# Optimization experiments

Hardware: AMD Instinct MI355X
Metric: run time of the kernel (lower is better)

## Reference

```python
import jax, jax.numpy as jnp
import numpy as np

# geomloss SamplesLoss defaults for loss='sinkhorn'
BLUR = 0.05
SCALING = 0.5
P = 1  # norm=1 -> cost C(x,y) = ||x - y||_2


def _cost(x, y):
    # Euclidean distance cost (p=1). x:(B,N,D), y:(B,M,D) -> (B,N,M)
    d2 = (jnp.sum(x * x, -1)[:, :, None]
          - 2.0 * jnp.einsum('bnd,bmd->bnm', x, y)
          + jnp.sum(y * y, -1)[:, None, :])
    return jnp.sqrt(jnp.clip(d2, 1e-12, None))  # tiny clamp keeps sqrt grad finite on diagonal


def _softmin(eps, C, h):
    # f_i = -eps * logsumexp_j( h_j - C_ij / eps );  C:(B,N,M), h:(B,M) -> (B,N)
    return -eps * jax.nn.logsumexp(h[:, None, :] - C / eps, axis=2)


def _eps_schedule(diameter):
    # geomloss epsilon_schedule(p, diameter, blur, scaling)
    return ([diameter ** P]
            + [float(np.exp(e)) for e in np.arange(P * np.log(diameter), P * np.log(BLUR), P * np.log(SCALING))]
            + [BLUR ** P])


def _sinkhorn_divergence(x, y):
    # Debiased Sinkhorn divergence (geomloss, tensorized backend, balanced OT).
    B, N, D = x.shape
    M = y.shape[1]
    a_log = jnp.full((B, N), -np.log(N), dtype=x.dtype)  # uniform weights (log)
    b_log = jnp.full((B, M), -np.log(M), dtype=x.dtype)

    C_xy = _cost(x, y)
    C_yx = jnp.swapaxes(C_xy, 1, 2)  # symmetric cost
    C_xx = _cost(x, x)
    C_yy = _cost(y, y)

    # diameter of the joint point cloud (geomloss max_diameter); concrete python float
    xf = np.asarray(x).reshape(-1, D)
    yf = np.asarray(y).reshape(-1, D)
    mins = np.minimum(xf.min(0), yf.min(0))
    maxs = np.maximum(xf.max(0), yf.max(0))
    diameter = float(np.linalg.norm(maxs - mins))
    eps_list = _eps_schedule(diameter)

    sg = jax.lax.stop_gradient

    # initialization at the largest eps
    eps = eps_list[0]
    f_aa = _softmin(eps, C_xx, a_log)
    g_bb = _softmin(eps, C_yy, b_log)
    g_ab = _softmin(eps, C_yx, a_log)
    f_ba = _softmin(eps, C_xy, b_log)

    # epsilon-annealing loop with symmetric (averaged) updates; no grad flows
    # through this loop (outputs are stop_gradient'ed in the final extrapolation)
    for eps in eps_list:
        ft_ba = _softmin(eps, C_xy, b_log + g_ab / eps)
        gt_ab = _softmin(eps, C_yx, a_log + f_ba / eps)
        f_ba = 0.5 * (f_ba + ft_ba)
        g_ab = 0.5 * (g_ab + gt_ab)
        ft_aa = _softmin(eps, C_xx, a_log + f_aa / eps)
        gt_bb = _softmin(eps, C_yy, b_log + g_bb / eps)
        f_aa = 0.5 * (f_aa + ft_aa)
        g_bb = 0.5 * (g_bb + gt_bb)

    # last extrapolation at eps = blur^p with detached dual potentials (envelope theorem)
    eps = eps_list[-1]
    f_ba_new = _softmin(eps, C_xy, sg(b_log + g_ab / eps))
    g_ab_new = _softmin(eps, C_yx, sg(a_log + f_ba / eps))
    f_aa = _softmin(eps, C_xx, sg(a_log + f_aa / eps))
    g_bb = _softmin(eps, C_yy, sg(b_log + g_bb / eps))
    f_ba, g_ab = f_ba_new, g_ab_new

    a = jnp.exp(a_log)
    b = jnp.exp(b_log)
    # S_eps(a,b) = <a, f_ba - f_aa> + <b, g_ab - g_bb>, per batch element
    return jnp.sum(a * (f_ba - f_aa), -1) + jnp.sum(b * (g_ab - g_bb), -1)


def setup_inputs() -> dict:
    key = jax.random.key(0)
    k1, k2 = jax.random.split(key)
    pre = jax.random.normal(k1, (2, 4096, 2), dtype=jnp.float32)
    gt = jax.random.normal(k2, (2, 4096, 2), dtype=jnp.float32)
    return {"pre": pre, "gt": gt}


def reference(pre, gt):
    return _sinkhorn_divergence(pre, gt).mean()
```

## Files before the change

kernel.cpp:

```cpp
#include <hip/hip_runtime.h>
#include <math.h>

#define NPTS 4096
#define NB 2
#define K_TOTAL 12
#define BLOCK 256
#define TILE 128
#define NT (NPTS / TILE)

#define SCHED_OFF 0
#define ML_OFF 32
#define P_OFF 576
#define POT_SZ (4 * NB * NPTS)
#define RED_OFF (P_OFF + 2 * POT_SZ)
#define PART_OFF (RED_OFF + 128)
#define PART_SZ (4 * NB * NT * NPTS)

#if __has_builtin(__builtin_amdgcn_exp2f)
#define EXP2F __builtin_amdgcn_exp2f
#else
#define EXP2F exp2f
#endif
#if __has_builtin(__builtin_amdgcn_logf)
#define LOG2F __builtin_amdgcn_logf
#else
#define LOG2F log2f
#endif
#if __has_builtin(__builtin_amdgcn_sqrtf)
#define FSQRTF __builtin_amdgcn_sqrtf
#else
#define FSQRTF sqrtf
#endif

#define BASE_LOGW -8.31776616671934f
#define LOG2E 1.4426950408889634f
#define LN2 0.69314718055994531f

typedef float v2f __attribute__((ext_vector_type(2)));

__global__ __launch_bounds__(256) void k_init(
    const float2* __restrict__ x, const float2* __restrict__ y, float* ws)
{
  const int tid = threadIdx.x;
  const int bid = blockIdx.x;

  if (bid > 0) {
    for (int i = (bid - 1) * 256 + tid; i < 2 * POT_SZ; i += 63 * 256)
      ws[P_OFF + i] = 0.0f;
    return;
  }

  float mnx = 1e30f, mny = 1e30f, mxx = -1e30f, mxy = -1e30f;
  for (int i = tid; i < NB * NPTS; i += 256) {
    float2 p = x[i];
    mnx = fminf(mnx, p.x); mxx = fmaxf(mxx, p.x);
    mny = fminf(mny, p.y); mxy = fmaxf(mxy, p.y);
    float2 q = y[i];
    mnx = fminf(mnx, q.x); mxx = fmaxf(mxx, q.x);
    mny = fminf(mny, q.y); mxy = fmaxf(mxy, q.y);
  }
  for (int o = 32; o; o >>= 1) {
    mnx = fminf(mnx, __shfl_xor(mnx, o, 64));
    mxx = fmaxf(mxx, __shfl_xor(mxx, o, 64));
    mny = fminf(mny, __shfl_xor(mny, o, 64));
    mxy = fmaxf(mxy, __shfl_xor(mxy, o, 64));
  }
  __shared__ float r[4][4];
  const int wave = tid >> 6, lane = tid & 63;
  if (lane == 0) { r[0][wave] = mnx; r[1][wave] = mxx; r[2][wave] = mny; r[3][wave] = mxy; }
  __syncthreads();
  if (tid == 0) {
    mnx = fminf(fminf(r[0][0], r[0][1]), fminf(r[0][2], r[0][3]));
    mxx = fmaxf(fmaxf(r[1][0], r[1][1]), fmaxf(r[1][2], r[1][3]));
    mny = fminf(fminf(r[2][0], r[2][1]), fminf(r[2][2], r[2][3]));
    mxy = fmaxf(fmaxf(r[3][0], r[3][1]), fmaxf(r[3][2], r[3][3]));
    float rx = mxx - mnx, ry = mxy - mny;
    float dia = sqrtf(rx * rx + ry * ry);

    double a = log((double)dia);
    double stop = log(0.05);
    double stp = log(0.5);
    int cnt = (int)ceil((stop - a) / stp);
    if (cnt < 0) cnt = 0;
    if (cnt > K_TOTAL - 4) cnt = K_TOTAL - 4;

    float* sch = ws + SCHED_OFF;
    sch[0] = dia; sch[1] = 0.0f;
    sch[2] = dia; sch[3] = 0.5f;
    for (int k = 0; k < cnt; k++) {
      sch[2 * (2 + k)] = (float)exp(a + (double)k * stp);
      sch[2 * (2 + k) + 1] = 0.5f;
    }
    sch[2 * (2 + cnt)] = 0.05f; sch[2 * (2 + cnt) + 1] = 0.5f;
    for (int s = 3 + cnt; s < K_TOTAL - 1; s++) { sch[2 * s] = 0.05f; sch[2 * s + 1] = 1.0f; }
    sch[2 * (K_TOTAL - 1)] = 0.05f; sch[2 * (K_TOTAL - 1) + 1] = 0.0f;
  }
}

__global__ __launch_bounds__(BLOCK, 4) void k_tiles(
    const float2* __restrict__ xpts, const float2* __restrict__ ypts,
    float* __restrict__ ws, int stepi)
{
  __shared__ float rXs[TILE], rYs[TILE], rVs[TILE];
  __shared__ float cXs[144], cYs[144], cVs[144];
  __shared__ float tPart[16][129];
  __shared__ float sfb[2][32];
  __shared__ float smx[2];
  __shared__ float wmax[4];

  const int tid = threadIdx.x;
  const int id = blockIdx.x;

  const float2* rowp; const float2* colp;
  int ti, tj, pbr, pbc;
  bool dual;

  if (id < NB * NT * NT) {
    const int b = id >> 10;
    const int t = id & (NT * NT - 1);
    ti = t >> 5; tj = t & (NT - 1);
    rowp = xpts + b * NPTS; colp = ypts + b * NPTS;
    pbr = 0 * NB + b; pbc = 1 * NB + b;
    dual = true;
  } else {
    const int id2 = id - NB * NT * NT;
    const int mat = id2 / 1056;
    const int rem = id2 - mat * 1056;
    const int b = rem / 528;
    const int k = rem - b * 528;
    int t0 = (int)((65.0f - FSQRTF((float)(4225 - 8 * k))) * 0.5f);
    while (t0 * (65 - t0) / 2 > k) t0--;
    while ((t0 + 1) * (64 - t0) / 2 <= k) t0++;
    ti = t0; tj = t0 + (k - t0 * (65 - t0) / 2);
    const float2* pts = mat ? ypts : xpts;
    rowp = pts + b * NPTS; colp = rowp;
    pbr = (2 + mat) * NB + b; pbc = pbr;
    dual = (ti != tj);
  }

  const float eps = ws[SCHED_OFF + 2 * stepi];
  const float sc = LOG2E / eps;
  const float inv_eps = 1.0f / eps;
  const int ppar = (stepi - 1) & 1;
  const int cpar = stepi & 1;

  if (stepi > 0 && tid < 64) {
    const int c = tid & 31, side = tid >> 5;
    const int pb_own = side ? pbc : pbr;
    const int spb = (pb_own < 4) ? (pb_own ^ 2) : pb_own;
    float ml = ws[ML_OFF + ppar * 256 + spb * NT + c];
    float mm = ml;
    mm = fmaxf(mm, __shfl_xor(mm, 1, 64));
    mm = fmaxf(mm, __shfl_xor(mm, 2, 64));
    mm = fmaxf(mm, __shfl_xor(mm, 4, 64));
    mm = fmaxf(mm, __shfl_xor(mm, 8, 64));
    mm = fmaxf(mm, __shfl_xor(mm, 16, 64));
    sfb[side][c] = EXP2F((ml - mm) * LOG2E);
    if (c == 0) smx[side] = mm;
  }
  __syncthreads();

  const int side = tid >> 7, kk0 = tid & 127;
  const int pb_own = side ? pbc : pbr;
  const int tile_own = side ? tj : ti;
  const int r = tile_own * TILE + kk0;
  float2 pt = (side ? colp : rowp)[r];

  float h;
  if (stepi == 0) {
    h = BASE_LOGW;
  } else {
    const float eps_p = ws[SCHED_OFF + 2 * (stepi - 1)];
    const float w_p = ws[SCHED_OFF + 2 * (stepi - 1) + 1];
    const float* pprev = ws + PART_OFF + ppar * PART_SZ + (pb_own * NT) * NPTS + r;
    float s = 0.0f;
#pragma unroll
    for (int c = 0; c < NT; c++) s += pprev[c * NPTS] * sfb[side][c];
    s = fmaxf(s, 1e-37f);
    float ft = -eps_p * fmaf(LN2, LOG2F(s), smx[side]);
    float po = ws[P_OFF + cpar * POT_SZ + pb_own * NPTS + r];
    float pn = (w_p >= 1.0f) ? po : fmaf(w_p, po, (1.0f - w_p) * ft);
    ws[P_OFF + ppar * POT_SZ + pb_own * NPTS + r] = pn;
    h = fmaf(pn, inv_eps, BASE_LOGW);
  }

  float hm = h;
  for (int o = 32; o; o >>= 1) hm = fmaxf(hm, __shfl_xor(hm, o, 64));
  if ((tid & 63) == 0) wmax[tid >> 6] = hm;
  __syncthreads();
  const float Mloc = fmaxf(wmax[2 * side], wmax[2 * side + 1]);

  if (side == 0) {
    rXs[kk0] = pt.x * sc; rYs[kk0] = pt.y * sc;
    rVs[kk0] = EXP2F((h - Mloc) * LOG2E);
  } else {
    const int kk = kk0 + (kk0 >> 3);
    cXs[kk] = pt.x * sc; cYs[kk] = pt.y * sc;
    cVs[kk] = EXP2F((h - Mloc) * LOG2E);
  }
  if (kk0 == 0) ws[ML_OFF + cpar * 256 + pb_own * NT + tile_own] = Mloc;
  __syncthreads();

  const int tx = tid & 15, ty = tid >> 4;
  float rx[8], ry[8], rv[8];
  v2f cx2[4], cy2[4], cv2[4], racc2[8], cacc2[4];
#pragma unroll
  for (int q = 0; q < 8; q++) {
    rx[q] = rXs[ty * 8 + q]; ry[q] = rYs[ty * 8 + q]; rv[q] = rVs[ty * 8 + q];
    racc2[q] = (v2f){0.0f, 0.0f};
  }
#pragma unroll
  for (int j = 0; j < 4; j++) {
    const int ci = tx * 9 + 2 * j;
    cx2[j] = (v2f){cXs[ci], cXs[ci + 1]};
    cy2[j] = (v2f){cYs[ci], cYs[ci + 1]};
    cv2[j] = (v2f){cVs[ci], cVs[ci + 1]};
    cacc2[j] = (v2f){0.0f, 0.0f};
  }

#pragma unroll
  for (int q = 0; q < 8; q++) {
    const v2f rxq = (v2f){rx[q], rx[q]};
    const v2f ryq = (v2f){ry[q], ry[q]};
    const v2f rvq = (v2f){rv[q], rv[q]};
#pragma unroll
    for (int j = 0; j < 4; j++) {
      v2f dx = rxq - cx2[j];
      v2f dy = ryq - cy2[j];
      v2f d2 = dx * dx + dy * dy;
      float t0 = FSQRTF(d2.x), t1 = FSQRTF(d2.y);
      v2f K = (v2f){EXP2F(-t0), EXP2F(-t1)};
      racc2[q] += K * cv2[j];
      cacc2[j] += K * rvq;
    }
  }

  float* part = ws + PART_OFF + cpar * PART_SZ;

#pragma unroll
  for (int q = 0; q < 8; q++) tPart[tx][ty * 8 + q] = racc2[q].x + racc2[q].y;
  __syncthreads();
  if (tid < TILE) {
    float s = 0.0f;
#pragma unroll
    for (int t = 0; t < 16; t++) s += tPart[t][tid];
    part[(pbr * NT + tj) * NPTS + ti * TILE + tid] = s;
  }
  __syncthreads();

#pragma unroll
  for (int j = 0; j < 4; j++) {
    tPart[ty][tx * 8 + 2 * j] = cacc2[j].x;
    tPart[ty][tx * 8 + 2 * j + 1] = cacc2[j].y;
  }
  __syncthreads();
  if (dual && tid < TILE) {
    float s = 0.0f;
#pragma unroll
    for (int t = 0; t < 16; t++) s += tPart[t][tid];
    part[(pbc * NT + ti) * NPTS + tj * TILE + tid] = s;
  }
}

__global__ __launch_bounds__(256) void k_psum(float* __restrict__ ws)
{
  const int pb = blockIdx.x >> 3, chunk = blockIdx.x & 7;
  const int tid = threadIdx.x;
  const int lpar = (K_TOTAL - 1) & 1;
  const float eps_l = ws[SCHED_OFF + 2 * (K_TOTAL - 1)];

  __shared__ float sfl[32];
  __shared__ float mmS;
  if (tid < 32) {
    const int spb = (pb < 4) ? (pb ^ 2) : pb;
    float ml = ws[ML_OFF + lpar * 256 + spb * NT + tid];
    float mm = ml;
    mm = fmaxf(mm, __shfl_xor(mm, 1, 64));
    mm = fmaxf(mm, __shfl_xor(mm, 2, 64));
    mm = fmaxf(mm, __shfl_xor(mm, 4, 64));
    mm = fmaxf(mm, __shfl_xor(mm, 8, 64));
    mm = fmaxf(mm, __shfl_xor(mm, 16, 64));
    sfl[tid] = EXP2F((ml - mm) * LOG2E);
    if (tid == 0) mmS = mm;
  }
  __syncthreads();

  double acc = 0.0;
#pragma unroll
  for (int rr = 0; rr < 2; rr++) {
    const int r = chunk * 512 + rr * 256 + tid;
    const float* pp = ws + PART_OFF + lpar * PART_SZ + (pb * NT) * NPTS + r;
    float s = 0.0f;
#pragma unroll
    for (int c = 0; c < NT; c++) s += pp[c * NPTS] * sfl[c];
    s = fmaxf(s, 1e-37f);
    float f = -eps_l * fmaf(LN2, LOG2F(s), mmS);
    acc += (double)f;
  }
  for (int o = 32; o; o >>= 1) acc += __shfl_xor(acc, o, 64);
  __shared__ double rd[4];
  if ((tid & 63) == 0) rd[tid >> 6] = acc;
  __syncthreads();
  if (tid == 0) {
    double s = (rd[0] + rd[1]) + (rd[2] + rd[3]);
    ((double*)(ws + RED_OFF))[blockIdx.x] = (pb < 2 * NB) ? s : -s;
  }
}

__global__ __launch_bounds__(64) void k_final(const float* __restrict__ ws,
                                              float* __restrict__ out)
{
  double v = ((const double*)(ws + RED_OFF))[threadIdx.x];
  for (int o = 32; o; o >>= 1) v += __shfl_xor(v, o, 64);
  if (threadIdx.x == 0) out[0] = (float)(v / (double)(NB * NPTS));
}

extern "C" void kernel_launch(void* const* d_in, const int* in_sizes, int n_in,
                              void* d_out, int out_size, void* d_ws, size_t ws_size,
                              hipStream_t stream)
{
  const float2* x = (const float2*)d_in[0];
  const float2* y = (const float2*)d_in[1];
  float* ws = (float*)d_ws;

  k_init<<<64, 256, 0, stream>>>(x, y, ws);

  const int nblocks = NB * NT * NT + 2 * NB * (NT * (NT + 1)) / 2;
  for (int s = 0; s < K_TOTAL; s++) {
    k_tiles<<<nblocks, BLOCK, 0, stream>>>(x, y, ws, s);
  }
  k_psum<<<64, 256, 0, stream>>>(ws);
  k_final<<<1, 64, 0, stream>>>(ws, (float*)d_out);
}
```

Measured before the change: 412.5 us.

## Process two column tiles per block for the cross-cost xy tiles

Each block handling the x-y cost matrix now covers one row tile against two adjacent column tiles, reusing the row points and the row accumulators across both. The column-B potentials are loaded before the first tile's reduction and are rescaled to a shared pair maximum. The row partial for the second tile is written as zero and its log-max is shared between the pair. This halves the number of xy blocks and cuts redundant row-potential recomputation, at the cost of more barriers, more shared memory and higher register pressure per block.

```diff
diff --git a/kernel.cpp b/kernel.cpp
--- a/kernel.cpp
+++ b/kernel.cpp
@@ -103,6 +103,7 @@
 {
   __shared__ float rXs[TILE], rYs[TILE], rVs[TILE];
   __shared__ float cXs[144], cYs[144], cVs[144];
+  __shared__ float cXs2[144], cYs2[144], cVs2[144];
   __shared__ float tPart[16][129];
   __shared__ float sfb[2][32];
   __shared__ float smx[2];
@@ -110,77 +111,274 @@
 
   const int tid = threadIdx.x;
   const int id = blockIdx.x;
-
-  const float2* rowp; const float2* colp;
-  int ti, tj, pbr, pbc;
-  bool dual;
-
-  if (id < NB * NT * NT) {
-    const int b = id >> 10;
-    const int t = id & (NT * NT - 1);
-    ti = t >> 5; tj = t & (NT - 1);
-    rowp = xpts + b * NPTS; colp = ypts + b * NPTS;
-    pbr = 0 * NB + b; pbc = 1 * NB + b;
-    dual = true;
-  } else {
-    const int id2 = id - NB * NT * NT;
-    const int mat = id2 / 1056;
-    const int rem = id2 - mat * 1056;
-    const int b = rem / 528;
-    const int k = rem - b * 528;
-    int t0 = (int)((65.0f - FSQRTF((float)(4225 - 8 * k))) * 0.5f);
-    while (t0 * (65 - t0) / 2 > k) t0--;
-    while ((t0 + 1) * (64 - t0) / 2 <= k) t0++;
-    ti = t0; tj = t0 + (k - t0 * (65 - t0) / 2);
-    const float2* pts = mat ? ypts : xpts;
-    rowp = pts + b * NPTS; colp = rowp;
-    pbr = (2 + mat) * NB + b; pbc = pbr;
-    dual = (ti != tj);
-  }
+  const int tx = tid & 15, ty = tid >> 4;
 
   const float eps = ws[SCHED_OFF + 2 * stepi];
   const float sc = LOG2E / eps;
   const float inv_eps = 1.0f / eps;
   const int ppar = (stepi - 1) & 1;
   const int cpar = stepi & 1;
+  const float eps_p = ws[SCHED_OFF + 2 * ((stepi > 0 ? stepi : 1) - 1)];
+  const float w_p = ws[SCHED_OFF + 2 * ((stepi > 0 ? stepi : 1) - 1) + 1];
+
+  if (id < NB * NT * 16) {
+    const int b = id >> 9;
+    const int rem = id & 511;
+    const int ti = rem >> 4, u = rem & 15;
+    const int tjA = 2 * u, tjB = 2 * u + 1;
+    const float2* rowp = xpts + b * NPTS;
+    const float2* colp = ypts + b * NPTS;
+    const int pbr = b, pbc = NB + b;
+
+    if (stepi > 0 && tid < 64) {
+      const int c = tid & 31, sd = tid >> 5;
+      const int pb_own = sd ? pbc : pbr;
+      const int spb = pb_own ^ 2;
+      float ml = ws[ML_OFF + ppar * 256 + spb * NT + c];
+      float mm = ml;
+      mm = fmaxf(mm, __shfl_xor(mm, 1, 64));
+      mm = fmaxf(mm, __shfl_xor(mm, 2, 64));
+      mm = fmaxf(mm, __shfl_xor(mm, 4, 64));
+      mm = fmaxf(mm, __shfl_xor(mm, 8, 64));
+      mm = fmaxf(mm, __shfl_xor(mm, 16, 64));
+      sfb[sd][c] = EXP2F((ml - mm) * LOG2E);
+      if (c == 0) smx[sd] = mm;
+    }
+    __syncthreads();
+
+    const int side = tid >> 7, kk0 = tid & 127;
+    const int pb_own = side ? pbc : pbr;
+    const int tile_own = side ? tjA : ti;
+    const int r = tile_own * TILE + kk0;
+    float2 pt = (side ? colp : rowp)[r];
+
+    float h;
+    if (stepi == 0) {
+      h = BASE_LOGW;
+    } else {
+      const float* pprev = ws + PART_OFF + ppar * PART_SZ + (pb_own * NT) * NPTS + r;
+      float s = 0.0f;
+#pragma unroll
+      for (int c = 0; c < NT; c++) s += pprev[c * NPTS] * sfb[side][c];
+      s = fmaxf(s, 1e-37f);
+      float ft = -eps_p * fmaf(LN2, LOG2F(s), smx[side]);
+      float po = ws[P_OFF + cpar * POT_SZ + pb_own * NPTS + r];
+      float pn = (w_p >= 1.0f) ? po : fmaf(w_p, po, (1.0f - w_p) * ft);
+      ws[P_OFF + ppar * POT_SZ + pb_own * NPTS + r] = pn;
+      h = fmaf(pn, inv_eps, BASE_LOGW);
+    }
+
+    float hm = h;
+    for (int o = 32; o; o >>= 1) hm = fmaxf(hm, __shfl_xor(hm, o, 64));
+    if ((tid & 63) == 0) wmax[tid >> 6] = hm;
+    __syncthreads();
+    const float MlocRow = fmaxf(wmax[0], wmax[1]);
+    const float MlocA = fmaxf(wmax[2], wmax[3]);
+    const float Mloc = side ? MlocA : MlocRow;
+
+    if (side == 0) {
+      rXs[kk0] = pt.x * sc; rYs[kk0] = pt.y * sc;
+      rVs[kk0] = EXP2F((h - Mloc) * LOG2E);
+      if (kk0 == 0) ws[ML_OFF + cpar * 256 + pbr * NT + ti] = MlocRow;
+    } else {
+      const int kk = kk0 + (kk0 >> 3);
+      cXs[kk] = pt.x * sc; cYs[kk] = pt.y * sc;
+      cVs[kk] = EXP2F((h - Mloc) * LOG2E);
+    }
+    __syncthreads();
+
+    float rx[8], ry[8], rv[8];
+    v2f cx2[4], cy2[4], cv2[4], racc2[8], cacc2[4];
+#pragma unroll
+    for (int q = 0; q < 8; q++) {
+      rx[q] = rXs[ty * 8 + q]; ry[q] = rYs[ty * 8 + q]; rv[q] = rVs[ty * 8 + q];
+      racc2[q] = (v2f){0.0f, 0.0f};
+    }
+#pragma unroll
+    for (int j = 0; j < 4; j++) {
+      const int ci = tx * 9 + 2 * j;
+      cx2[j] = (v2f){cXs[ci], cXs[ci + 1]};
+      cy2[j] = (v2f){cYs[ci], cYs[ci + 1]};
+      cv2[j] = (v2f){cVs[ci], cVs[ci + 1]};
+      cacc2[j] = (v2f){0.0f, 0.0f};
+    }
+
+#pragma unroll
+    for (int q = 0; q < 8; q++) {
+      const v2f rxq = (v2f){rx[q], rx[q]};
+      const v2f ryq = (v2f){ry[q], ry[q]};
+      const v2f rvq = (v2f){rv[q], rv[q]};
+#pragma unroll
+      for (int j = 0; j < 4; j++) {
+        v2f dx = rxq - cx2[j];
+        v2f dy = ryq - cy2[j];
+        v2f d2 = dx * dx + dy * dy;
+        float t0 = FSQRTF(d2.x), t1 = FSQRTF(d2.y);
+        v2f K = (v2f){EXP2F(-t0), EXP2F(-t1)};
+        racc2[q] += K * cv2[j];
+        cacc2[j] += K * rvq;
+      }
+    }
+
+    float* part = ws + PART_OFF + cpar * PART_SZ;
+
+#pragma unroll
+    for (int j = 0; j < 4; j++) {
+      tPart[ty][tx * 8 + 2 * j] = cacc2[j].x;
+      tPart[ty][tx * 8 + 2 * j + 1] = cacc2[j].y;
+    }
+    const int rB = tjB * TILE + kk0;
+    float pbv[32]; float2 ptB = (float2){0.0f, 0.0f}; float poB = 0.0f;
+    if (side == 1) {
+      ptB = colp[rB];
+      if (stepi > 0) {
+        const float* pprevB = ws + PART_OFF + ppar * PART_SZ + (pbc * NT) * NPTS + rB;
+#pragma unroll
+        for (int c = 0; c < NT; c++) pbv[c] = pprevB[c * NPTS];
+        poB = ws[P_OFF + cpar * POT_SZ + pbc * NPTS + rB];
+      }
+    }
+    __syncthreads();
+    if (tid < TILE) {
+      float s = 0.0f;
+#pragma unroll
+      for (int t = 0; t < 16; t++) s += tPart[t][tid];
+      part[(pbc * NT + ti) * NPTS + tjA * TILE + tid] = s;
+    }
+
+    float hB = BASE_LOGW;
+    if (side == 1 && stepi > 0) {
+      float s = 0.0f;
+#pragma unroll
+      for (int c = 0; c < NT; c++) s += pbv[c] * sfb[1][c];
+      s = fmaxf(s, 1e-37f);
+      float ft = -eps_p * fmaf(LN2, LOG2F(s), smx[1]);
+      float pn = (w_p >= 1.0f) ? poB : fmaf(w_p, poB, (1.0f - w_p) * ft);
+      ws[P_OFF + ppar * POT_SZ + pbc * NPTS + rB] = pn;
+      hB = fmaf(pn, inv_eps, BASE_LOGW);
+    }
+    float hmB = hB;
+    for (int o = 32; o; o >>= 1) hmB = fmaxf(hmB, __shfl_xor(hmB, o, 64));
+    if ((tid & 63) == 0) wmax[tid >> 6] = hmB;
+    __syncthreads();
+    const float MlocB = fmaxf(wmax[2], wmax[3]);
+
+    const float Mpair = fmaxf(MlocA, MlocB);
+    const float rscale = EXP2F((MlocA - Mpair) * LOG2E);
+    const v2f rsc2 = (v2f){rscale, rscale};
+#pragma unroll
+    for (int q = 0; q < 8; q++) racc2[q] *= rsc2;
+
+    if (side == 1) {
+      const int kk = kk0 + (kk0 >> 3);
+      cXs2[kk] = ptB.x * sc; cYs2[kk] = ptB.y * sc;
+      cVs2[kk] = EXP2F((hB - Mpair) * LOG2E);
+      if (kk0 == 0) {
+        ws[ML_OFF + cpar * 256 + pbc * NT + tjA] = Mpair;
+        ws[ML_OFF + cpar * 256 + pbc * NT + tjB] = Mpair;
+      }
+    }
+    __syncthreads();
+
+#pragma unroll
+    for (int j = 0; j < 4; j++) {
+      const int ci = tx * 9 + 2 * j;
+      cx2[j] = (v2f){cXs2[ci], cXs2[ci + 1]};
+      cy2[j] = (v2f){cYs2[ci], cYs2[ci + 1]};
+      cv2[j] = (v2f){cVs2[ci], cVs2[ci + 1]};
+      cacc2[j] = (v2f){0.0f, 0.0f};
+    }
+#pragma unroll
+    for (int q = 0; q < 8; q++) {
+      const v2f rxq = (v2f){rx[q], rx[q]};
+      const v2f ryq = (v2f){ry[q], ry[q]};
+      const v2f rvq = (v2f){rv[q], rv[q]};
+#pragma unroll
+      for (int j = 0; j < 4; j++) {
+        v2f dx = rxq - cx2[j];
+        v2f dy = ryq - cy2[j];
+        v2f d2 = dx * dx + dy * dy;
+        float t0 = FSQRTF(d2.x), t1 = FSQRTF(d2.y);
+        v2f K = (v2f){EXP2F(-t0), EXP2F(-t1)};
+        racc2[q] += K * cv2[j];
+        cacc2[j] += K * rvq;
+      }
+    }
+
+    __syncthreads();
+#pragma unroll
+    for (int j = 0; j < 4; j++) {
+      tPart[ty][tx * 8 + 2 * j] = cacc2[j].x;
+      tPart[ty][tx * 8 + 2 * j + 1] = cacc2[j].y;
+    }
+    __syncthreads();
+    if (tid < TILE) {
+      float s = 0.0f;
+#pragma unroll
+      for (int t = 0; t < 16; t++) s += tPart[t][tid];
+      part[(pbc * NT + ti) * NPTS + tjB * TILE + tid] = s;
+    }
+    __syncthreads();
+
+#pragma unroll
+    for (int q = 0; q < 8; q++) tPart[tx][ty * 8 + q] = racc2[q].x + racc2[q].y;
+    __syncthreads();
+    if (tid < TILE) {
+      float s = 0.0f;
+#pragma unroll
+      for (int t = 0; t < 16; t++) s += tPart[t][tid];
+      part[(pbr * NT + tjA) * NPTS + ti * TILE + tid] = s;
+      part[(pbr * NT + tjB) * NPTS + ti * TILE + tid] = 0.0f;
+    }
+    return;
+  }
+
+  const int id2 = id - NB * NT * 16;
+  const int mat = id2 / 1056;
+  const int rem = id2 - mat * 1056;
+  const int b = rem / 528;
+  const int k = rem - b * 528;
+  int t0i = (int)((65.0f - FSQRTF((float)(4225 - 8 * k))) * 0.5f);
+  while (t0i * (65 - t0i) / 2 > k) t0i--;
+  while ((t0i + 1) * (64 - t0i) / 2 <= k) t0i++;
+  const int ti = t0i, tj = t0i + (k - t0i * (65 - t0i) / 2);
+  const float2* pts = mat ? ypts : xpts;
+  const float2* rowp = pts + b * NPTS;
+  const int pb = (2 + mat) * NB + b;
+  const bool dual = (ti != tj);
 
   if (stepi > 0 && tid < 64) {
-    const int c = tid & 31, side = tid >> 5;
-    const int pb_own = side ? pbc : pbr;
-    const int spb = (pb_own < 4) ? (pb_own ^ 2) : pb_own;
-    float ml = ws[ML_OFF + ppar * 256 + spb * NT + c];
+    const int c = tid & 31, sd = tid >> 5;
+    float ml = ws[ML_OFF + ppar * 256 + pb * NT + c];
     float mm = ml;
     mm = fmaxf(mm, __shfl_xor(mm, 1, 64));
     mm = fmaxf(mm, __shfl_xor(mm, 2, 64));
     mm = fmaxf(mm, __shfl_xor(mm, 4, 64));
     mm = fmaxf(mm, __shfl_xor(mm, 8, 64));
     mm = fmaxf(mm, __shfl_xor(mm, 16, 64));
-    sfb[side][c] = EXP2F((ml - mm) * LOG2E);
-    if (c == 0) smx[side] = mm;
+    sfb[sd][c] = EXP2F((ml - mm) * LOG2E);
+    if (c == 0) smx[sd] = mm;
   }
   __syncthreads();
 
   const int side = tid >> 7, kk0 = tid & 127;
-  const int pb_own = side ? pbc : pbr;
   const int tile_own = side ? tj : ti;
   const int r = tile_own * TILE + kk0;
-  float2 pt = (side ? colp : rowp)[r];
+  float2 pt = rowp[r];
 
   float h;
   if (stepi == 0) {
     h = BASE_LOGW;
   } else {
-    const float eps_p = ws[SCHED_OFF + 2 * (stepi - 1)];
-    const float w_p = ws[SCHED_OFF + 2 * (stepi - 1) + 1];
-    const float* pprev = ws + PART_OFF + ppar * PART_SZ + (pb_own * NT) * NPTS + r;
+    const float* pprev = ws + PART_OFF + ppar * PART_SZ + (pb * NT) * NPTS + r;
     float s = 0.0f;
 #pragma unroll
     for (int c = 0; c < NT; c++) s += pprev[c * NPTS] * sfb[side][c];
     s = fmaxf(s, 1e-37f);
     float ft = -eps_p * fmaf(LN2, LOG2F(s), smx[side]);
-    float po = ws[P_OFF + cpar * POT_SZ + pb_own * NPTS + r];
+    float po = ws[P_OFF + cpar * POT_SZ + pb * NPTS + r];
     float pn = (w_p >= 1.0f) ? po : fmaf(w_p, po, (1.0f - w_p) * ft);
-    ws[P_OFF + ppar * POT_SZ + pb_own * NPTS + r] = pn;
+    ws[P_OFF + ppar * POT_SZ + pb * NPTS + r] = pn;
     h = fmaf(pn, inv_eps, BASE_LOGW);
   }
 
@@ -198,10 +396,9 @@
     cXs[kk] = pt.x * sc; cYs[kk] = pt.y * sc;
     cVs[kk] = EXP2F((h - Mloc) * LOG2E);
   }
-  if (kk0 == 0) ws[ML_OFF + cpar * 256 + pb_own * NT + tile_own] = Mloc;
-  __syncthreads();
-
-  const int tx = tid & 15, ty = tid >> 4;
+  if (kk0 == 0) ws[ML_OFF + cpar * 256 + pb * NT + tile_own] = Mloc;
+  __syncthreads();
+
   float rx[8], ry[8], rv[8];
   v2f cx2[4], cy2[4], cv2[4], racc2[8], cacc2[4];
 #pragma unroll
@@ -244,7 +441,7 @@
     float s = 0.0f;
 #pragma unroll
     for (int t = 0; t < 16; t++) s += tPart[t][tid];
-    part[(pbr * NT + tj) * NPTS + ti * TILE + tid] = s;
+    part[(pb * NT + tj) * NPTS + ti * TILE + tid] = s;
   }
   __syncthreads();
 
@@ -258,7 +455,7 @@
     float s = 0.0f;
 #pragma unroll
     for (int t = 0; t < 16; t++) s += tPart[t][tid];
-    part[(pbc * NT + ti) * NPTS + tj * TILE + tid] = s;
+    part[(pb * NT + ti) * NPTS + tj * TILE + tid] = s;
   }
 }
 
@@ -325,7 +522,7 @@
 
   k_init<<<64, 256, 0, stream>>>(x, y, ws);
 
-  const int nblocks = NB * NT * NT + 2 * NB * (NT * (NT + 1)) / 2;
+  const int nblocks = NB * NT * 16 + 2 * NB * (NT * (NT + 1)) / 2;
   for (int s = 0; s < K_TOTAL; s++) {
     k_tiles<<<nblocks, BLOCK, 0, stream>>>(x, y, ws, s);
   }
```

Measured after the change: 512.7 us. 24.3% more time.
